# Performance work log

Measured on AMD Instinct MI355X. Metric: run time of the kernel, lower is better.

Reference implementation:

```python
import jax, jax.numpy as jnp
import numpy as np

S, B, D, E, H, REQ = 2048, 4, 256, 256, 8, 16  # seq, batch, hidden_dim, embed(=hidden_size), heads, band half-width


def setup_inputs() -> dict:
    key = jax.random.key(0)
    ks = jax.random.split(key, 12)
    w = lambda k, shape: jax.random.normal(k, shape, jnp.float32) * 0.02
    return {
        "mod": jax.random.normal(ks[0], (S, B, D), jnp.float32),
        "mask": jnp.zeros((B, S), jnp.float32),  # unused in speaker=False branch (kept for fidelity)
        "Wq": w(ks[1], (E, D)), "bq": jnp.zeros((E,), jnp.float32),
        "Wk": w(ks[2], (E, D)), "bk": jnp.zeros((E,), jnp.float32),
        "Wv": w(ks[3], (E, D)), "bv": jnp.zeros((E,), jnp.float32),
        "Win": w(ks[4], (3 * E, E)), "bin_": jnp.zeros((3 * E,), jnp.float32),  # MHA in_proj
        "Wout": w(ks[5], (E, E)), "bout": jnp.zeros((E,), jnp.float32),         # MHA out_proj
        "Wfc": w(ks[6], (D, E)), "bfc": jnp.zeros((D,), jnp.float32),           # self.fc
        "gamma": jnp.ones((D,), jnp.float32), "beta": jnp.zeros((D,), jnp.float32),
        "req": REQ,
    }


def reference(mod, mask, Wq, bq, Wk, bk, Wv, bv, Win, bin_, Wout, bout, Wfc, bfc, gamma, beta, req):
    s, b, d = mod.shape
    e = Wq.shape[0]
    hd = e // H
    # fc_q/k/v (pre-projection) then MultiheadAttention's own in_proj
    q = mod @ Wq.T + bq                       # (s, b, e)
    k = mod @ Wk.T + bk
    v = mod @ Wv.T + bv
    q = q @ Win[:e].T + bin_[:e]
    k = k @ Win[e:2 * e].T + bin_[e:2 * e]
    v = v @ Win[2 * e:].T + bin_[2 * e:]
    split = lambda x: x.reshape(s, b, H, hd).transpose(1, 2, 0, 3)  # (b, H, s, hd)
    qh, kh, vh = split(q), split(k), split(v)
    scores = jnp.einsum('bhqd,bhkd->bhqk', qh, kh) / jnp.sqrt(jnp.float32(hd))
    idx = jnp.arange(s)
    allowed = jnp.abs(idx[:, None] - idx[None, :]) < req  # band: diag + offsets 1..req-1
    scores = jnp.where(allowed[None, None], scores, -jnp.inf)
    attn = jax.nn.softmax(scores, axis=-1)                # attn dropout = identity (eval)
    ctx = jnp.einsum('bhqk,bhkd->bhqd', attn, vh)
    ctx = ctx.transpose(2, 0, 1, 3).reshape(s, b, e)
    ctx = ctx @ Wout.T + bout
    y = ctx @ Wfc.T + bfc + mod                           # dropout(0.5) = identity (eval), residual
    mu = jnp.mean(y, axis=-1, keepdims=True)
    var = jnp.var(y, axis=-1, keepdims=True)
    return (y - mu) / jnp.sqrt(var + 1e-6) * gamma + beta
```

## Files before the change

### kernel.cpp

```cpp
#include <hip/hip_runtime.h>
#include <hip/hip_bf16.h>
#include <math.h>

#define SS 2048
#define BB 4
#define DD 256
#define EE 256
#define HH 8
#define HD 32
#define TT (SS*BB)

typedef unsigned short ushortt;
typedef __attribute__((ext_vector_type(8))) short short8;
typedef __attribute__((ext_vector_type(4))) float f32x4;

__device__ __forceinline__ float bfbits2f(ushortt u) {
    return __uint_as_float(((unsigned int)u) << 16);
}
__device__ __forceinline__ ushortt f2bf_bits(float f) {
    unsigned int u = __float_as_uint(f);
    unsigned int r = u + 0x7FFFu + ((u >> 16) & 1u);
    return (ushortt)(r >> 16);
}

__device__ __forceinline__ int robust_req(const void* p) {
    int i = *(const int*)p;
    if (i >= 1 && i <= SS) return i;
    float f = __int_as_float(i);
    if (f >= 1.f && f <= (float)SS) return (int)(f + 0.5f);
    float b = bfbits2f(*(const ushortt*)p);
    if (b >= 1.f && b <= (float)SS) return (int)(b + 0.5f);
    return 16;
}

__global__ void f32_to_bf16(const float* __restrict__ in, ushortt* __restrict__ out, int n) {
    int i = (blockIdx.x * blockDim.x + threadIdx.x) * 4;
    if (i + 3 < n) {
        float4 v = *(const float4*)(in + i);
        ushort4 o;
        o.x = f2bf_bits(v.x); o.y = f2bf_bits(v.y);
        o.z = f2bf_bits(v.z); o.w = f2bf_bits(v.w);
        *(ushort4*)(out + i) = o;
    }
}

__global__ void fuse_w_qkv(const float* __restrict__ Win,
                           const float* __restrict__ Wq,
                           const float* __restrict__ Wk,
                           const float* __restrict__ Wv,
                           const float* __restrict__ bq,
                           const float* __restrict__ bk,
                           const float* __restrict__ bv,
                           const float* __restrict__ bin_,
                           ushortt* __restrict__ Weffb,
                           float* __restrict__ beff) {
    int r = blockIdx.x;
    int d = threadIdx.x;
    int i = r / EE;
    const float* Wi = (i == 0) ? Wq : ((i == 1) ? Wk : Wv);
    const float* bi = (i == 0) ? bq : ((i == 1) ? bk : bv);
    float acc = 0.f;
    for (int e1 = 0; e1 < EE; ++e1) acc += Win[r * EE + e1] * Wi[e1 * DD + d];
    Weffb[(size_t)r * DD + d] = f2bf_bits(acc);
    float tb = Win[r * EE + d] * bi[d];
#pragma unroll
    for (int off = 32; off >= 1; off >>= 1) tb += __shfl_xor(tb, off);
    __shared__ float red[4];
    if ((d & 63) == 0) red[d >> 6] = tb;
    __syncthreads();
    if (d == 0) beff[r] = red[0] + red[1] + red[2] + red[3] + bin_[r];
}

__global__ void fuse_w_out(const float* __restrict__ Wfc,
                           const float* __restrict__ Wout,
                           const float* __restrict__ bout,
                           const float* __restrict__ bfc,
                           ushortt* __restrict__ W2b,
                           float* __restrict__ b2) {
    int d  = blockIdx.x;
    int e2 = threadIdx.x;
    float acc = 0.f;
    for (int e = 0; e < EE; ++e) acc += Wfc[d * EE + e] * Wout[e * EE + e2];
    W2b[(size_t)d * EE + e2] = f2bf_bits(acc);
    float tb = Wfc[d * EE + e2] * bout[e2];
#pragma unroll
    for (int off = 32; off >= 1; off >>= 1) tb += __shfl_xor(tb, off);
    __shared__ float red[4];
    if ((e2 & 63) == 0) red[e2 >> 6] = tb;
    __syncthreads();
    if (e2 == 0) b2[d] = red[0] + red[1] + red[2] + red[3] + bfc[d];
}

template<int EPI>
__global__ __launch_bounds__(256)
void gemm_mfma(const ushortt* __restrict__ A, const ushortt* __restrict__ Bw,
               const float* __restrict__ bias, const float* __restrict__ res,
               void* __restrict__ Cout, int M, int N, int K) {
    __shared__ __align__(16) ushortt Alds[128][40];
    __shared__ __align__(16) ushortt Blds[64][40];
    const int t    = threadIdx.x;
    const int lane = t & 63;
    const int w    = t >> 6;
    const int wm   = w >> 1, wn = w & 1;
    const int quad = lane >> 4;
    const int l16  = lane & 15;
    const int m0   = blockIdx.y * 128;
    const int n0   = blockIdx.x * 64;

    f32x4 acc[4][2];
#pragma unroll
    for (int fm = 0; fm < 4; ++fm)
#pragma unroll
        for (int fn = 0; fn < 2; ++fn) acc[fm][fn] = (f32x4){0.f, 0.f, 0.f, 0.f};

    const int sr = t >> 2;
    const int sp = (t & 3) * 8;

    for (int k0 = 0; k0 < K; k0 += 32) {
        *(float4*)&Alds[sr][sp]      = *(const float4*)(A + (size_t)(m0 + sr) * K + k0 + sp);
        *(float4*)&Alds[sr + 64][sp] = *(const float4*)(A + (size_t)(m0 + sr + 64) * K + k0 + sp);
        *(float4*)&Blds[sr][sp]      = *(const float4*)(Bw + (size_t)(n0 + sr) * K + k0 + sp);
        __syncthreads();
        short8 af[4], bfr[2];
#pragma unroll
        for (int fm = 0; fm < 4; ++fm)
            af[fm] = *(const short8*)&Alds[wm * 64 + fm * 16 + l16][quad * 8];
#pragma unroll
        for (int fn = 0; fn < 2; ++fn)
            bfr[fn] = *(const short8*)&Blds[wn * 32 + fn * 16 + l16][quad * 8];
#pragma unroll
        for (int fm = 0; fm < 4; ++fm)
#pragma unroll
            for (int fn = 0; fn < 2; ++fn)
                acc[fm][fn] = __builtin_amdgcn_mfma_f32_16x16x32_bf16(
                    af[fm], bfr[fn], acc[fm][fn], 0, 0, 0);
        __syncthreads();
    }
#pragma unroll
    for (int fm = 0; fm < 4; ++fm) {
#pragma unroll
        for (int fn = 0; fn < 2; ++fn) {
#pragma unroll
            for (int r = 0; r < 4; ++r) {
                int row = m0 + wm * 64 + fm * 16 + quad * 4 + r;
                int col = n0 + wn * 32 + fn * 16 + l16;
                float v = acc[fm][fn][r] + bias[col];
                if (EPI == 1) {
                    ((float*)Cout)[(size_t)row * N + col] = v + res[(size_t)row * N + col];
                } else {
                    ((ushortt*)Cout)[(size_t)row * N + col] = f2bf_bits(v);
                }
            }
        }
    }
}

__global__ __launch_bounds__(256)
void attn_mfma(const ushortt* __restrict__ qkv,
               const void* __restrict__ reqp,
               ushortt* __restrict__ ctx) {
    __shared__ __align__(16) ushortt Plds[4][16 * 72];
    const int t    = threadIdx.x;
    const int w    = t >> 6;
    const int lane = t & 63;
    const int l16  = lane & 15;
    const int quad = lane >> 4;
    const int wid  = blockIdx.x * 4 + w;
    const int stile = wid >> 5;
    const int rem   = wid & 31;
    const int b = rem >> 3;
    const int h = rem & 7;
    const int s0 = stile * 16;
    const int req = robust_req(reqp);

    const ushortt* qptr = qkv + ((size_t)(s0 + l16) * BB + b) * (3 * EE) + h * HD + quad * 8;
    short8 aq = *(const short8*)qptr;

    f32x4 sc[3];
#pragma unroll
    for (int kt = 0; kt < 3; ++kt) {
        int j = s0 - 16 + kt * 16 + l16;
        int jc = min(max(j, 0), SS - 1);
        const ushortt* kp = qkv + ((size_t)jc * BB + b) * (3 * EE) + EE + h * HD + quad * 8;
        short8 bk = *(const short8*)kp;
        sc[kt] = __builtin_amdgcn_mfma_f32_16x16x32_bf16(aq, bk, (f32x4){0.f,0.f,0.f,0.f}, 0, 0, 0);
    }

    const float scale = 0.17677669529663687f;
    float pv[3][4];
#pragma unroll
    for (int r = 0; r < 4; ++r) {
        int s = s0 + quad * 4 + r;
        float vv[3];
        float mx = -INFINITY;
#pragma unroll
        for (int kt = 0; kt < 3; ++kt) {
            int j = s0 - 16 + kt * 16 + l16;
            int dj = s - j;
            bool valid = (j >= 0) && (j < SS) && (dj < req) && (-dj < req);
            vv[kt] = valid ? sc[kt][r] * scale : -INFINITY;
            mx = fmaxf(mx, vv[kt]);
        }
#pragma unroll
        for (int off = 1; off <= 8; off <<= 1) mx = fmaxf(mx, __shfl_xor(mx, off));
        float sum = 0.f;
#pragma unroll
        for (int kt = 0; kt < 3; ++kt) {
            float p = (vv[kt] > -INFINITY) ? __expf(vv[kt] - mx) : 0.f;
            pv[kt][r] = p;
            sum += p;
        }
#pragma unroll
        for (int off = 1; off <= 8; off <<= 1) sum += __shfl_xor(sum, off);
        float inv = 1.f / sum;
#pragma unroll
        for (int kt = 0; kt < 3; ++kt) pv[kt][r] *= inv;
    }

    ushortt* P = &Plds[w][0];
#pragma unroll
    for (int kt = 0; kt < 3; ++kt)
#pragma unroll
        for (int r = 0; r < 4; ++r)
            P[(quad * 4 + r) * 72 + kt * 16 + l16] = f2bf_bits(pv[kt][r]);
#pragma unroll
    for (int r = 0; r < 4; ++r)
        P[(quad * 4 + r) * 72 + 48 + l16] = 0;
    __syncthreads();

    short8 pa[2];
    pa[0] = *(const short8*)&P[l16 * 72 + quad * 8];
    pa[1] = *(const short8*)&P[l16 * 72 + 32 + quad * 8];

    f32x4 acc[2];
    acc[0] = (f32x4){0.f,0.f,0.f,0.f};
    acc[1] = (f32x4){0.f,0.f,0.f,0.f};
#pragma unroll
    for (int c = 0; c < 2; ++c) {
#pragma unroll
        for (int nd = 0; nd < 2; ++nd) {
            short8 bv;
#pragma unroll
            for (int u = 0; u < 8; ++u) {
                int j = s0 - 16 + c * 32 + quad * 8 + u;
                int jc = min(max(j, 0), SS - 1);
                bv[u] = (short)qkv[((size_t)jc * BB + b) * (3 * EE) + 2 * EE + h * HD + nd * 16 + l16];
            }
            acc[nd] = __builtin_amdgcn_mfma_f32_16x16x32_bf16(pa[c], bv, acc[nd], 0, 0, 0);
        }
    }

#pragma unroll
    for (int nd = 0; nd < 2; ++nd)
#pragma unroll
        for (int r = 0; r < 4; ++r) {
            int tok = (s0 + quad * 4 + r) * BB + b;
            ctx[(size_t)tok * EE + h * HD + nd * 16 + l16] = f2bf_bits(acc[nd][r]);
        }
}

__global__ void ln_kernel(float* __restrict__ y,
                          const float* __restrict__ gamma,
                          const float* __restrict__ beta) {
    int t = blockIdx.x, d = threadIdx.x;
    float v = y[(size_t)t * DD + d];
    float s1 = v, s2 = v * v;
#pragma unroll
    for (int off = 32; off >= 1; off >>= 1) {
        s1 += __shfl_xor(s1, off);
        s2 += __shfl_xor(s2, off);
    }
    __shared__ float r1[4], r2[4];
    int w = threadIdx.x >> 6;
    if ((threadIdx.x & 63) == 0) { r1[w] = s1; r2[w] = s2; }
    __syncthreads();
    float S1 = r1[0] + r1[1] + r1[2] + r1[3];
    float S2 = r2[0] + r2[1] + r2[2] + r2[3];
    float mean = S1 * (1.f / DD);
    float var  = S2 * (1.f / DD) - mean * mean;
    float inv  = rsqrtf(var + 1e-6f);
    y[(size_t)t * DD + d] = (v - mean) * inv * gamma[d] + beta[d];
}

extern "C" void kernel_launch(void* const* d_in, const int* in_sizes, int n_in,
                              void* d_out, int out_size, void* d_ws, size_t ws_size,
                              hipStream_t stream) {
    const float* mod  = (const float*)d_in[0];
    const float* Wq   = (const float*)d_in[2];
    const float* bq   = (const float*)d_in[3];
    const float* Wk   = (const float*)d_in[4];
    const float* bk   = (const float*)d_in[5];
    const float* Wv   = (const float*)d_in[6];
    const float* bv   = (const float*)d_in[7];
    const float* Win  = (const float*)d_in[8];
    const float* bin_ = (const float*)d_in[9];
    const float* Wout = (const float*)d_in[10];
    const float* bout = (const float*)d_in[11];
    const float* Wfc  = (const float*)d_in[12];
    const float* bfc  = (const float*)d_in[13];
    const float* gamma= (const float*)d_in[14];
    const float* beta = (const float*)d_in[15];
    const void*  reqp = d_in[16];

    float* out = (float*)d_out;

    float*  beff = (float*)d_ws;
    float*  b2   = beff + 3 * EE;
    ushortt* Weffb = (ushortt*)(b2 + DD);
    ushortt* W2b   = Weffb + 3 * EE * DD;
    ushortt* modb  = W2b + DD * EE;
    ushortt* qkvb  = modb + (size_t)TT * DD;
    ushortt* ctxb  = qkvb + (size_t)TT * 3 * EE;

    f32_to_bf16<<<(TT * DD / 4 + 255) / 256, 256, 0, stream>>>(mod, modb, TT * DD);
    fuse_w_qkv<<<3 * EE, DD, 0, stream>>>(Win, Wq, Wk, Wv, bq, bk, bv, bin_, Weffb, beff);
    fuse_w_out<<<DD, EE, 0, stream>>>(Wfc, Wout, bout, bfc, W2b, b2);
    gemm_mfma<0><<<dim3(3 * EE / 64, TT / 128), 256, 0, stream>>>(
        modb, Weffb, beff, nullptr, qkvb, TT, 3 * EE, DD);
    attn_mfma<<<4096 / 4, 256, 0, stream>>>(qkvb, reqp, ctxb);
    gemm_mfma<1><<<dim3(DD / 64, TT / 128), 256, 0, stream>>>(
        ctxb, W2b, b2, mod, out, TT, DD, EE);
    ln_kernel<<<TT, DD, 0, stream>>>(out, gamma, beta);
}
```

Baseline: 152.2 us.

## Fuse bf16 conversion into QKV GEMM, merge weight-fusion kernels, fuse LayerNorm into tail GEMM

Removes the separate fp32-to-bf16 pass over the input by converting rows on the fly while loading them into LDS in the QKV GEMM. The two weight-folding kernels become one launch. The output GEMM is restructured so each block owns 64 full rows across all 256 columns, letting it add bias and residual and apply LayerNorm in registers. This drops a full fp32 write and read of the output and two launches. In exchange, the QKV GEMM now reads fp32 activations once per column tile, and the tail GEMM has fewer blocks (128) and more accumulator registers.

```diff
diff --git a/kernel.cpp b/kernel.cpp
--- a/kernel.cpp
+++ b/kernel.cpp
@@ -33,69 +33,50 @@
     return 16;
 }
 
-__global__ void f32_to_bf16(const float* __restrict__ in, ushortt* __restrict__ out, int n) {
-    int i = (blockIdx.x * blockDim.x + threadIdx.x) * 4;
-    if (i + 3 < n) {
-        float4 v = *(const float4*)(in + i);
-        ushort4 o;
-        o.x = f2bf_bits(v.x); o.y = f2bf_bits(v.y);
-        o.z = f2bf_bits(v.z); o.w = f2bf_bits(v.w);
-        *(ushort4*)(out + i) = o;
-    }
-}
-
-__global__ void fuse_w_qkv(const float* __restrict__ Win,
-                           const float* __restrict__ Wq,
-                           const float* __restrict__ Wk,
-                           const float* __restrict__ Wv,
-                           const float* __restrict__ bq,
-                           const float* __restrict__ bk,
-                           const float* __restrict__ bv,
-                           const float* __restrict__ bin_,
-                           ushortt* __restrict__ Weffb,
-                           float* __restrict__ beff) {
-    int r = blockIdx.x;
-    int d = threadIdx.x;
-    int i = r / EE;
-    const float* Wi = (i == 0) ? Wq : ((i == 1) ? Wk : Wv);
-    const float* bi = (i == 0) ? bq : ((i == 1) ? bk : bv);
-    float acc = 0.f;
-    for (int e1 = 0; e1 < EE; ++e1) acc += Win[r * EE + e1] * Wi[e1 * DD + d];
-    Weffb[(size_t)r * DD + d] = f2bf_bits(acc);
-    float tb = Win[r * EE + d] * bi[d];
-#pragma unroll
-    for (int off = 32; off >= 1; off >>= 1) tb += __shfl_xor(tb, off);
+__global__ __launch_bounds__(256)
+void fuse_weights(const float* __restrict__ Win,
+                  const float* __restrict__ Wq, const float* __restrict__ Wk,
+                  const float* __restrict__ Wv,
+                  const float* __restrict__ bq, const float* __restrict__ bk,
+                  const float* __restrict__ bv, const float* __restrict__ bin_,
+                  const float* __restrict__ Wfc, const float* __restrict__ Wout,
+                  const float* __restrict__ bout, const float* __restrict__ bfc,
+                  ushortt* __restrict__ Weffb, float* __restrict__ beff,
+                  ushortt* __restrict__ W2b, float* __restrict__ b2) {
     __shared__ float red[4];
-    if ((d & 63) == 0) red[d >> 6] = tb;
-    __syncthreads();
-    if (d == 0) beff[r] = red[0] + red[1] + red[2] + red[3] + bin_[r];
-}
-
-__global__ void fuse_w_out(const float* __restrict__ Wfc,
-                           const float* __restrict__ Wout,
-                           const float* __restrict__ bout,
-                           const float* __restrict__ bfc,
-                           ushortt* __restrict__ W2b,
-                           float* __restrict__ b2) {
-    int d  = blockIdx.x;
-    int e2 = threadIdx.x;
-    float acc = 0.f;
-    for (int e = 0; e < EE; ++e) acc += Wfc[d * EE + e] * Wout[e * EE + e2];
-    W2b[(size_t)d * EE + e2] = f2bf_bits(acc);
-    float tb = Wfc[d * EE + e2] * bout[e2];
-#pragma unroll
-    for (int off = 32; off >= 1; off >>= 1) tb += __shfl_xor(tb, off);
-    __shared__ float red[4];
-    if ((e2 & 63) == 0) red[e2 >> 6] = tb;
-    __syncthreads();
-    if (e2 == 0) b2[d] = red[0] + red[1] + red[2] + red[3] + bfc[d];
-}
-
-template<int EPI>
+    int t = threadIdx.x;
+    if (blockIdx.x < 3 * EE) {
+        int r = blockIdx.x;
+        int i = r / EE;
+        const float* Wi = (i == 0) ? Wq : ((i == 1) ? Wk : Wv);
+        const float* bi = (i == 0) ? bq : ((i == 1) ? bk : bv);
+        float acc = 0.f;
+        for (int e1 = 0; e1 < EE; ++e1) acc += Win[r * EE + e1] * Wi[e1 * DD + t];
+        Weffb[(size_t)r * DD + t] = f2bf_bits(acc);
+        float tb = Win[r * EE + t] * bi[t];
+#pragma unroll
+        for (int off = 32; off >= 1; off >>= 1) tb += __shfl_xor(tb, off);
+        if ((t & 63) == 0) red[t >> 6] = tb;
+        __syncthreads();
+        if (t == 0) beff[r] = red[0] + red[1] + red[2] + red[3] + bin_[r];
+    } else {
+        int d = blockIdx.x - 3 * EE;
+        float acc = 0.f;
+        for (int e = 0; e < EE; ++e) acc += Wfc[d * EE + e] * Wout[e * EE + t];
+        W2b[(size_t)d * EE + t] = f2bf_bits(acc);
+        float tb = Wfc[d * EE + t] * bout[t];
+#pragma unroll
+        for (int off = 32; off >= 1; off >>= 1) tb += __shfl_xor(tb, off);
+        if ((t & 63) == 0) red[t >> 6] = tb;
+        __syncthreads();
+        if (t == 0) b2[d] = red[0] + red[1] + red[2] + red[3] + bfc[d];
+    }
+}
+
 __global__ __launch_bounds__(256)
-void gemm_mfma(const ushortt* __restrict__ A, const ushortt* __restrict__ Bw,
-               const float* __restrict__ bias, const float* __restrict__ res,
-               void* __restrict__ Cout, int M, int N, int K) {
+void gemm_qkv(const float* __restrict__ A, const ushortt* __restrict__ Bw,
+              const float* __restrict__ bias, ushortt* __restrict__ C,
+              int M, int N, int K) {
     __shared__ __align__(16) ushortt Alds[128][40];
     __shared__ __align__(16) ushortt Blds[64][40];
     const int t    = threadIdx.x;
@@ -117,9 +98,20 @@
     const int sp = (t & 3) * 8;
 
     for (int k0 = 0; k0 < K; k0 += 32) {
-        *(float4*)&Alds[sr][sp]      = *(const float4*)(A + (size_t)(m0 + sr) * K + k0 + sp);
-        *(float4*)&Alds[sr + 64][sp] = *(const float4*)(A + (size_t)(m0 + sr + 64) * K + k0 + sp);
-        *(float4*)&Blds[sr][sp]      = *(const float4*)(Bw + (size_t)(n0 + sr) * K + k0 + sp);
+#pragma unroll
+        for (int half = 0; half < 2; ++half) {
+            const float* ap = A + (size_t)(m0 + sr + half * 64) * K + k0 + sp;
+            float4 v0 = *(const float4*)ap;
+            float4 v1 = *(const float4*)(ap + 4);
+            ushort4 o0, o1;
+            o0.x = f2bf_bits(v0.x); o0.y = f2bf_bits(v0.y);
+            o0.z = f2bf_bits(v0.z); o0.w = f2bf_bits(v0.w);
+            o1.x = f2bf_bits(v1.x); o1.y = f2bf_bits(v1.y);
+            o1.z = f2bf_bits(v1.z); o1.w = f2bf_bits(v1.w);
+            *(ushort4*)&Alds[sr + half * 64][sp]     = o0;
+            *(ushort4*)&Alds[sr + half * 64][sp + 4] = o1;
+        }
+        *(float4*)&Blds[sr][sp] = *(const float4*)(Bw + (size_t)(n0 + sr) * K + k0 + sp);
         __syncthreads();
         short8 af[4], bfr[2];
 #pragma unroll
@@ -137,22 +129,15 @@
         __syncthreads();
     }
 #pragma unroll
-    for (int fm = 0; fm < 4; ++fm) {
-#pragma unroll
-        for (int fn = 0; fn < 2; ++fn) {
+    for (int fm = 0; fm < 4; ++fm)
+#pragma unroll
+        for (int fn = 0; fn < 2; ++fn)
 #pragma unroll
             for (int r = 0; r < 4; ++r) {
                 int row = m0 + wm * 64 + fm * 16 + quad * 4 + r;
                 int col = n0 + wn * 32 + fn * 16 + l16;
-                float v = acc[fm][fn][r] + bias[col];
-                if (EPI == 1) {
-                    ((float*)Cout)[(size_t)row * N + col] = v + res[(size_t)row * N + col];
-                } else {
-                    ((ushortt*)Cout)[(size_t)row * N + col] = f2bf_bits(v);
-                }
-            }
-        }
-    }
+                C[(size_t)row * N + col] = f2bf_bits(acc[fm][fn][r] + bias[col]);
+            }
 }
 
 __global__ __launch_bounds__(256)
@@ -259,27 +244,96 @@
         }
 }
 
-__global__ void ln_kernel(float* __restrict__ y,
-                          const float* __restrict__ gamma,
-                          const float* __restrict__ beta) {
-    int t = blockIdx.x, d = threadIdx.x;
-    float v = y[(size_t)t * DD + d];
-    float s1 = v, s2 = v * v;
-#pragma unroll
-    for (int off = 32; off >= 1; off >>= 1) {
-        s1 += __shfl_xor(s1, off);
-        s2 += __shfl_xor(s2, off);
-    }
-    __shared__ float r1[4], r2[4];
-    int w = threadIdx.x >> 6;
-    if ((threadIdx.x & 63) == 0) { r1[w] = s1; r2[w] = s2; }
+__global__ __launch_bounds__(256)
+void gemm_tail_ln(const ushortt* __restrict__ A, const ushortt* __restrict__ Bw,
+                  const float* __restrict__ b2, const float* __restrict__ mod,
+                  const float* __restrict__ gamma, const float* __restrict__ beta,
+                  float* __restrict__ out) {
+    __shared__ __align__(16) ushortt Alds[64][40];
+    __shared__ __align__(16) ushortt Blds[256][40];
+    __shared__ float part1[4][64], part2[4][64];
+    const int t    = threadIdx.x;
+    const int lane = t & 63;
+    const int wn   = t >> 6;
+    const int quad = lane >> 4;
+    const int l16  = lane & 15;
+    const int m0   = blockIdx.x * 64;
+    const int N    = DD, K = EE;
+
+    f32x4 acc[4][4];
+#pragma unroll
+    for (int fm = 0; fm < 4; ++fm)
+#pragma unroll
+        for (int fn = 0; fn < 4; ++fn) acc[fm][fn] = (f32x4){0.f, 0.f, 0.f, 0.f};
+
+    const int sr = t >> 2;
+    const int sp = (t & 3) * 8;
+
+    for (int k0 = 0; k0 < K; k0 += 32) {
+        *(float4*)&Alds[sr][sp] = *(const float4*)(A + (size_t)(m0 + sr) * K + k0 + sp);
+#pragma unroll
+        for (int i = 0; i < 4; ++i)
+            *(float4*)&Blds[sr + i * 64][sp] = *(const float4*)(Bw + (size_t)(sr + i * 64) * K + k0 + sp);
+        __syncthreads();
+        short8 af[4], bfr[4];
+#pragma unroll
+        for (int fm = 0; fm < 4; ++fm)
+            af[fm] = *(const short8*)&Alds[fm * 16 + l16][quad * 8];
+#pragma unroll
+        for (int fn = 0; fn < 4; ++fn)
+            bfr[fn] = *(const short8*)&Blds[wn * 64 + fn * 16 + l16][quad * 8];
+#pragma unroll
+        for (int fm = 0; fm < 4; ++fm)
+#pragma unroll
+            for (int fn = 0; fn < 4; ++fn)
+                acc[fm][fn] = __builtin_amdgcn_mfma_f32_16x16x32_bf16(
+                    af[fm], bfr[fn], acc[fm][fn], 0, 0, 0);
+        __syncthreads();
+    }
+
+#pragma unroll
+    for (int fm = 0; fm < 4; ++fm) {
+#pragma unroll
+        for (int r = 0; r < 4; ++r) {
+            int rowl = fm * 16 + quad * 4 + r;
+            int row  = m0 + rowl;
+            float s1 = 0.f, s2 = 0.f;
+#pragma unroll
+            for (int fn = 0; fn < 4; ++fn) {
+                int col = wn * 64 + fn * 16 + l16;
+                float v = acc[fm][fn][r] + b2[col] + mod[(size_t)row * N + col];
+                acc[fm][fn][r] = v;
+                s1 += v;
+                s2 += v * v;
+            }
+#pragma unroll
+            for (int off = 1; off <= 8; off <<= 1) {
+                s1 += __shfl_xor(s1, off);
+                s2 += __shfl_xor(s2, off);
+            }
+            if (l16 == 0) { part1[wn][rowl] = s1; part2[wn][rowl] = s2; }
+        }
+    }
     __syncthreads();
-    float S1 = r1[0] + r1[1] + r1[2] + r1[3];
-    float S2 = r2[0] + r2[1] + r2[2] + r2[3];
-    float mean = S1 * (1.f / DD);
-    float var  = S2 * (1.f / DD) - mean * mean;
-    float inv  = rsqrtf(var + 1e-6f);
-    y[(size_t)t * DD + d] = (v - mean) * inv * gamma[d] + beta[d];
+#pragma unroll
+    for (int fm = 0; fm < 4; ++fm) {
+#pragma unroll
+        for (int r = 0; r < 4; ++r) {
+            int rowl = fm * 16 + quad * 4 + r;
+            int row  = m0 + rowl;
+            float S1 = part1[0][rowl] + part1[1][rowl] + part1[2][rowl] + part1[3][rowl];
+            float S2 = part2[0][rowl] + part2[1][rowl] + part2[2][rowl] + part2[3][rowl];
+            float mean = S1 * (1.f / DD);
+            float var  = S2 * (1.f / DD) - mean * mean;
+            float inv  = rsqrtf(var + 1e-6f);
+#pragma unroll
+            for (int fn = 0; fn < 4; ++fn) {
+                int col = wn * 64 + fn * 16 + l16;
+                out[(size_t)row * N + col] =
+                    (acc[fm][fn][r] - mean) * inv * gamma[col] + beta[col];
+            }
+        }
+    }
 }
 
 extern "C" void kernel_launch(void* const* d_in, const int* in_sizes, int n_in,
@@ -308,17 +362,14 @@
     float*  b2   = beff + 3 * EE;
     ushortt* Weffb = (ushortt*)(b2 + DD);
     ushortt* W2b   = Weffb + 3 * EE * DD;
-    ushortt* modb  = W2b + DD * EE;
-    ushortt* qkvb  = modb + (size_t)TT * DD;
+    ushortt* qkvb  = W2b + DD * EE;
     ushortt* ctxb  = qkvb + (size_t)TT * 3 * EE;
 
-    f32_to_bf16<<<(TT * DD / 4 + 255) / 256, 256, 0, stream>>>(mod, modb, TT * DD);
-    fuse_w_qkv<<<3 * EE, DD, 0, stream>>>(Win, Wq, Wk, Wv, bq, bk, bv, bin_, Weffb, beff);
-    fuse_w_out<<<DD, EE, 0, stream>>>(Wfc, Wout, bout, bfc, W2b, b2);
-    gemm_mfma<0><<<dim3(3 * EE / 64, TT / 128), 256, 0, stream>>>(
-        modb, Weffb, beff, nullptr, qkvb, TT, 3 * EE, DD);
+    fuse_weights<<<4 * EE, 256, 0, stream>>>(Win, Wq, Wk, Wv, bq, bk, bv, bin_,
+                                             Wfc, Wout, bout, bfc,
+                                             Weffb, beff, W2b, b2);
+    gemm_qkv<<<dim3(3 * EE / 64, TT / 128), 256, 0, stream>>>(
+        mod, Weffb, beff, qkvb, TT, 3 * EE, DD);
     attn_mfma<<<4096 / 4, 256, 0, stream>>>(qkvb, reqp, ctxb);
-    gemm_mfma<1><<<dim3(DD / 64, TT / 128), 256, 0, stream>>>(
-        ctxb, W2b, b2, mod, out, TT, DD, EE);
-    ln_kernel<<<TT, DD, 0, stream>>>(out, gamma, beta);
-}
+    gemm_tail_ln<<<TT / 64, 256, 0, stream>>>(ctxb, W2b, b2, mod, gamma, beta, out);
+}
```

Result: faster. 141.1 us (-7.3%).
